# Optimization experiments

Measured on AMD Instinct MI355X. Metric: run time of the kernel, lower is better.

## Reference

```python
import jax, jax.numpy as jnp
import numpy as np

D_MODEL = 1024
NUM_HEADS = 16
D_HEAD = D_MODEL // NUM_HEADS


def setup_inputs() -> dict:
    key = jax.random.key(0)
    ks = jax.random.split(key, 5)
    B, T = 4, 2048
    x = jax.random.normal(ks[0], (B, T, D_MODEL), dtype=jnp.float32)
    s = 1.0 / np.sqrt(D_MODEL)
    # torch nn.Linear params: weight [out, in], bias [out]
    qkv_w = jax.random.uniform(ks[1], (3 * D_MODEL, D_MODEL), jnp.float32, -s, s)
    qkv_b = jax.random.uniform(ks[2], (3 * D_MODEL,), jnp.float32, -s, s)
    out_w = jax.random.uniform(ks[3], (D_MODEL, D_MODEL), jnp.float32, -s, s)
    out_b = jax.random.uniform(ks[4], (D_MODEL,), jnp.float32, -s, s)
    return {"x": x, "qkv_w": qkv_w, "qkv_b": qkv_b, "out_w": out_w, "out_b": out_b}


def reference(x, qkv_w, qkv_b, out_w, out_b):
    B, T, D = x.shape
    H, dh = NUM_HEADS, D_HEAD
    qkv = x @ qkv_w.T + qkv_b                      # [B,T,3D]
    q, k, v = jnp.split(qkv, 3, axis=-1)           # each [B,T,D]
    # split heads -> [B,H,T,dh]
    q = q.reshape(B, T, H, dh).transpose(0, 2, 1, 3)
    k = k.reshape(B, T, H, dh).transpose(0, 2, 1, 3)
    v = v.reshape(B, T, H, dh).transpose(0, 2, 1, 3)
    scores = jnp.einsum('bhqd,bhkd->bhqk', q, k) / jnp.sqrt(jnp.float32(dh))
    attn = jax.nn.softmax(scores, axis=-1)         # dropout p=0 (eval)
    out = jnp.einsum('bhqk,bhkd->bhqd', attn, v)   # [B,H,T,dh]
    out = out.transpose(0, 2, 1, 3).reshape(B, T, D)
    return out @ out_w.T + out_b
```

## Files before the change

### kernel.cpp

```cpp
#include <hip/hip_runtime.h>
#include <hip/hip_bf16.h>

typedef __bf16 bf16;
typedef __bf16 bf16x4 __attribute__((ext_vector_type(4)));
typedef __bf16 bf16x8 __attribute__((ext_vector_type(8)));
typedef float floatx4 __attribute__((ext_vector_type(4)));

#define MFMA16(a, b, c) __builtin_amdgcn_mfma_f32_16x16x32_bf16((a), (b), (c), 0, 0, 0)

constexpr int NHEADS = 16;

__device__ __forceinline__ void gld16(const bf16* g, bf16* l) {
  __builtin_amdgcn_global_load_lds(
      (const __attribute__((address_space(1))) void*)g,
      (__attribute__((address_space(3))) void*)l, 16, 0, 0);
}

__global__ __launch_bounds__(256) void cvt_bf16(const float* __restrict__ src,
                                                bf16* __restrict__ dst) {
  const int i = blockIdx.x * 256 + threadIdx.x;
  floatx4 a = ((const floatx4*)src)[2 * i];
  floatx4 b = ((const floatx4*)src)[2 * i + 1];
  bf16x8 o = {(bf16)a[0], (bf16)a[1], (bf16)a[2], (bf16)a[3],
              (bf16)b[0], (bf16)b[1], (bf16)b[2], (bf16)b[3]};
  ((bf16x8*)dst)[i] = o;
}

template <int MODE>
__global__ __launch_bounds__(256) void gemm_bt(
    const bf16* __restrict__ A, const bf16* __restrict__ W,
    const float* __restrict__ bias, bf16* __restrict__ out0,
    bf16* __restrict__ out1, bf16* __restrict__ out2,
    float* __restrict__ outf) {
  __shared__ __attribute__((aligned(16))) bf16 lds_a[128 * 32];
  __shared__ __attribute__((aligned(16))) bf16 lds_b[128 * 32];

  const int tid = threadIdx.x;
  const int wid = tid >> 6;
  const int lane = tid & 63;
  const int quad = lane >> 4;
  const int l16 = lane & 15;
  const int block_m = blockIdx.y * 128;
  const int block_n = blockIdx.x * 128;
  const int wm = (wid >> 1) * 64;
  const int wn = (wid & 1) * 64;

  floatx4 acc[4][4];
#pragma unroll
  for (int i = 0; i < 4; ++i)
#pragma unroll
    for (int j = 0; j < 4; ++j) acc[i][j] = (floatx4){0.f, 0.f, 0.f, 0.f};

  for (int k0 = 0; k0 < 1024; k0 += 32) {
#pragma unroll
    for (int i = 0; i < 2; ++i) {
      const int slot = wid * 128 + i * 64 + lane;
      const int row = slot >> 2;
      const int blk = slot & 3;
      const int lbase = (wid * 128 + i * 64) * 8;
      gld16(&A[(size_t)(block_m + row) * 1024 + k0 + blk * 8], &lds_a[lbase]);
      gld16(&W[(size_t)(block_n + row) * 1024 + k0 + blk * 8], &lds_b[lbase]);
    }
    __syncthreads();

    bf16x8 af[4], bf_[4];
#pragma unroll
    for (int mt = 0; mt < 4; ++mt)
      af[mt] = *(const bf16x8*)&lds_a[(wm + mt * 16 + l16) * 32 + quad * 8];
#pragma unroll
    for (int nt = 0; nt < 4; ++nt)
      bf_[nt] = *(const bf16x8*)&lds_b[(wn + nt * 16 + l16) * 32 + quad * 8];
#pragma unroll
    for (int mt = 0; mt < 4; ++mt)
#pragma unroll
      for (int nt = 0; nt < 4; ++nt)
        acc[mt][nt] = MFMA16(af[mt], bf_[nt], acc[mt][nt]);
    __syncthreads();
  }

#pragma unroll
  for (int nt = 0; nt < 4; ++nt) {
    const int n = block_n + wn + nt * 16 + l16;
    const float bv = bias[n];
#pragma unroll
    for (int mt = 0; mt < 4; ++mt) {
#pragma unroll
      for (int r = 0; r < 4; ++r) {
        const int m = block_m + wm + mt * 16 + quad * 4 + r;
        const float v = acc[mt][nt][r] + bv;
        if constexpr (MODE == 1) {
          outf[(size_t)m * 1024 + n] = v;
        } else {
          const int which = n >> 10;
          const int d = n & 1023;
          const int h = d >> 6;
          const int dd = d & 63;
          const int b = m >> 11;
          const int t = m & 2047;
          const size_t bh = (size_t)(b * NHEADS + h);
          if (which == 0)
            out0[(bh * 2048 + t) * 64 + dd] = (bf16)v;
          else if (which == 1)
            out1[(bh * 2048 + t) * 64 + dd] = (bf16)v;
          else
            out2[(bh * 64 + dd) * 2048 + t] = (bf16)v;
        }
      }
    }
  }
}

__global__ __launch_bounds__(256) void flash_attn(
    const bf16* __restrict__ q, const bf16* __restrict__ k,
    const bf16* __restrict__ vt, bf16* __restrict__ ctx) {
  __shared__ __attribute__((aligned(16))) bf16 k_lds[2][64 * 64];
  __shared__ __attribute__((aligned(16))) bf16 v_lds[2][64 * 64];
  __shared__ __attribute__((aligned(16))) bf16 p_lds[4][32][72];

  const int tid = threadIdx.x;
  const int wid = tid >> 6;
  const int lane = tid & 63;
  const int quad = lane >> 4;
  const int l16 = lane & 15;
  const int b = blockIdx.z;
  const int h = blockIdx.y;
  const int q0 = blockIdx.x * 128;
  const size_t bh = (size_t)(b * NHEADS + h);
  const bf16* qb = q + bh * 2048 * 64;
  const bf16* kb = k + bh * 2048 * 64;
  const bf16* vb = vt + bh * 64 * 2048;

  const bf16x8 ones = {(bf16)1.f, (bf16)1.f, (bf16)1.f, (bf16)1.f,
                       (bf16)1.f, (bf16)1.f, (bf16)1.f, (bf16)1.f};

  const int slot0 = wid * 128 + lane;
  const int slot1 = slot0 + 64;
  const int row0 = slot0 >> 3, c0 = (slot0 & 7) ^ (row0 & 7);
  const int row1 = slot1 >> 3, c1 = (slot1 & 7) ^ (row1 & 7);
  const bf16* kst0 = kb + (size_t)row0 * 64 + c0 * 8;
  const bf16* kst1 = kb + (size_t)row1 * 64 + c1 * 8;
  const bf16* vst0 = vb + (size_t)row0 * 2048 + c0 * 8;
  const bf16* vst1 = vb + (size_t)row1 * 2048 + c1 * 8;
  const int ldst0 = wid * 1024;
  const int ldst1 = wid * 1024 + 512;

  const int r7 = l16 & 7;
  const int ro = l16 * 64;
  const int sw0 = ro + ((quad ^ r7) * 8);
  const int sw1 = ro + (((quad + 4) ^ r7) * 8);

  bf16x8 qa[2][2];
#pragma unroll
  for (int s = 0; s < 2; ++s) {
    const int row = q0 + wid * 32 + s * 16 + l16;
    qa[s][0] = *(const bf16x8*)&qb[(size_t)row * 64 + quad * 8];
    qa[s][1] = *(const bf16x8*)&qb[(size_t)row * 64 + 32 + quad * 8];
  }

  floatx4 oacc[2][4];
  floatx4 lacc[2];
#pragma unroll
  for (int s = 0; s < 2; ++s) {
    lacc[s] = (floatx4){0.f, 0.f, 0.f, 0.f};
#pragma unroll
    for (int dt = 0; dt < 4; ++dt) oacc[s][dt] = (floatx4){0.f, 0.f, 0.f, 0.f};
  }

  gld16(kst0, &k_lds[0][ldst0]);
  gld16(kst1, &k_lds[0][ldst1]);
  gld16(vst0, &v_lds[0][ldst0]);
  gld16(vst1, &v_lds[0][ldst1]);
  __syncthreads();

  constexpr float L2E = 1.4426950408889634f;
  int cur = 0;
  for (int kt = 0; kt < 2048; kt += 64) {
    if (kt + 64 < 2048) {
      const int nb = cur ^ 1;
      gld16(kst0 + (size_t)(kt + 64) * 64, &k_lds[nb][ldst0]);
      gld16(kst1 + (size_t)(kt + 64) * 64, &k_lds[nb][ldst1]);
      gld16(vst0 + (kt + 64), &v_lds[nb][ldst0]);
      gld16(vst1 + (kt + 64), &v_lds[nb][ldst1]);
    }

    const bf16* kbuf = &k_lds[cur][0];
    const bf16* vbuf = &v_lds[cur][0];
    bf16x8 kf0[4], kf1[4], vf0[4], vf1[4];
#pragma unroll
    for (int nt = 0; nt < 4; ++nt) {
      kf0[nt] = *(const bf16x8*)&kbuf[nt * 1024 + sw0];
      kf1[nt] = *(const bf16x8*)&kbuf[nt * 1024 + sw1];
    }
#pragma unroll
    for (int dt = 0; dt < 4; ++dt) {
      vf0[dt] = *(const bf16x8*)&vbuf[dt * 1024 + sw0];
      vf1[dt] = *(const bf16x8*)&vbuf[dt * 1024 + sw1];
    }

#pragma unroll
    for (int s = 0; s < 2; ++s) {
      floatx4 st[4];
#pragma unroll
      for (int nt = 0; nt < 4; ++nt) {
        floatx4 a0 = (floatx4){0.f, 0.f, 0.f, 0.f};
        a0 = MFMA16(qa[s][0], kf0[nt], a0);
        st[nt] = MFMA16(qa[s][1], kf1[nt], a0);
      }
#pragma unroll
      for (int nt = 0; nt < 4; ++nt)
#pragma unroll
        for (int r = 0; r < 4; ++r) {
          const float p =
              __builtin_amdgcn_exp2f(fmaf(st[nt][r], 0.125f * L2E, -3.0f * L2E));
          p_lds[wid][s * 16 + quad * 4 + r][nt * 16 + l16] = (bf16)p;
        }
    }

#pragma unroll
    for (int s = 0; s < 2; ++s) {
      bf16x8 pa0 = *(const bf16x8*)&p_lds[wid][s * 16 + l16][quad * 8];
      bf16x8 pa1 = *(const bf16x8*)&p_lds[wid][s * 16 + l16][32 + quad * 8];
#pragma unroll
      for (int dt = 0; dt < 4; ++dt) {
        oacc[s][dt] = MFMA16(pa0, vf0[dt], oacc[s][dt]);
        oacc[s][dt] = MFMA16(pa1, vf1[dt], oacc[s][dt]);
      }
      lacc[s] = MFMA16(pa0, ones, lacc[s]);
      lacc[s] = MFMA16(pa1, ones, lacc[s]);
    }

    __syncthreads();
    cur ^= 1;
  }

#pragma unroll
  for (int s = 0; s < 2; ++s) {
    float linv[4];
#pragma unroll
    for (int r = 0; r < 4; ++r) linv[r] = 1.f / lacc[s][r];
    const size_t base =
        ((size_t)b * 2048 + q0 + wid * 32 + s * 16) * 1024 + h * 64;
#pragma unroll
    for (int dt = 0; dt < 4; ++dt)
#pragma unroll
      for (int r = 0; r < 4; ++r) {
        const float v = oacc[s][dt][r] * linv[r];
        ctx[base + (size_t)(quad * 4 + r) * 1024 + dt * 16 + l16] = (bf16)v;
      }
  }
}

extern "C" void kernel_launch(void* const* d_in, const int* in_sizes, int n_in,
                              void* d_out, int out_size, void* d_ws,
                              size_t ws_size, hipStream_t stream) {
  const float* x = (const float*)d_in[0];
  const float* qkv_w = (const float*)d_in[1];
  const float* qkv_b = (const float*)d_in[2];
  const float* out_w = (const float*)d_in[3];
  const float* out_b = (const float*)d_in[4];
  float* out = (float*)d_out;

  bf16* xb = (bf16*)d_out;

  bf16* ws = (bf16*)d_ws;
  const size_t SZ = (size_t)8192 * 1024;
  bf16* qkvwb = ws;
  bf16* outwb = qkvwb + 3072 * 1024;
  bf16* qws = outwb + 1024 * 1024;
  bf16* kws = qws + SZ;
  bf16* vtws = kws + SZ;
  bf16* ctx = vtws + SZ;

  cvt_bf16<<<4096, 256, 0, stream>>>(x, xb);
  cvt_bf16<<<1536, 256, 0, stream>>>(qkv_w, qkvwb);
  cvt_bf16<<<512, 256, 0, stream>>>(out_w, outwb);

  gemm_bt<0><<<dim3(24, 64), 256, 0, stream>>>(xb, qkvwb, qkv_b, qws, kws,
                                               vtws, nullptr);
  flash_attn<<<dim3(16, 16, 4), 256, 0, stream>>>(qws, kws, vtws, ctx);
  gemm_bt<1><<<dim3(8, 64), 256, 0, stream>>>(ctx, outwb, out_b, nullptr,
                                              nullptr, nullptr, out);
}
```

Measured before the change: 316.4 us.

## Triple-buffer K/V loads in flash attention and remap blocks for XCD locality

```diff
diff --git a/kernel.cpp b/kernel.cpp
--- a/kernel.cpp
+++ b/kernel.cpp
@@ -113,8 +113,8 @@
 __global__ __launch_bounds__(256) void flash_attn(
     const bf16* __restrict__ q, const bf16* __restrict__ k,
     const bf16* __restrict__ vt, bf16* __restrict__ ctx) {
-  __shared__ __attribute__((aligned(16))) bf16 k_lds[2][64 * 64];
-  __shared__ __attribute__((aligned(16))) bf16 v_lds[2][64 * 64];
+  __shared__ __attribute__((aligned(16))) bf16 k_lds[3][64 * 64];
+  __shared__ __attribute__((aligned(16))) bf16 v_lds[3][64 * 64];
   __shared__ __attribute__((aligned(16))) bf16 p_lds[4][32][72];
 
   const int tid = threadIdx.x;
@@ -122,9 +122,12 @@
   const int lane = tid & 63;
   const int quad = lane >> 4;
   const int l16 = lane & 15;
-  const int b = blockIdx.z;
-  const int h = blockIdx.y;
-  const int q0 = blockIdx.x * 128;
+
+  const int wg = blockIdx.x;
+  const int nl = (wg & 7) * 128 + (wg >> 3);
+  const int q0 = (nl & 15) * 128;
+  const int h = (nl >> 4) & 15;
+  const int b = nl >> 8;
   const size_t bh = (size_t)(b * NHEADS + h);
   const bf16* qb = q + bh * 2048 * 64;
   const bf16* kb = k + bh * 2048 * 64;
@@ -170,18 +173,34 @@
   gld16(kst1, &k_lds[0][ldst1]);
   gld16(vst0, &v_lds[0][ldst0]);
   gld16(vst1, &v_lds[0][ldst1]);
-  __syncthreads();
+  gld16(kst0 + (size_t)64 * 64, &k_lds[1][ldst0]);
+  gld16(kst1 + (size_t)64 * 64, &k_lds[1][ldst1]);
+  gld16(vst0 + 64, &v_lds[1][ldst0]);
+  gld16(vst1 + 64, &v_lds[1][ldst1]);
 
   constexpr float L2E = 1.4426950408889634f;
-  int cur = 0;
-  for (int kt = 0; kt < 2048; kt += 64) {
-    if (kt + 64 < 2048) {
-      const int nb = cur ^ 1;
-      gld16(kst0 + (size_t)(kt + 64) * 64, &k_lds[nb][ldst0]);
-      gld16(kst1 + (size_t)(kt + 64) * 64, &k_lds[nb][ldst1]);
-      gld16(vst0 + (kt + 64), &v_lds[nb][ldst0]);
-      gld16(vst1 + (kt + 64), &v_lds[nb][ldst1]);
-    }
+  for (int t = 0; t < 32; ++t) {
+    const int kt = t * 64;
+    const int cur = t % 3;
+    if (t + 2 < 32) {
+      const int nb = (t + 2) % 3;
+      const size_t ko = (size_t)(kt + 128) * 64;
+      gld16(kst0 + ko, &k_lds[nb][ldst0]);
+      gld16(kst1 + ko, &k_lds[nb][ldst1]);
+      gld16(vst0 + (kt + 128), &v_lds[nb][ldst0]);
+      gld16(vst1 + (kt + 128), &v_lds[nb][ldst1]);
+    }
+
+    if (t < 30) {
+      asm volatile("s_waitcnt vmcnt(8)" ::: "memory");
+    } else if (t == 30) {
+      asm volatile("s_waitcnt vmcnt(4)" ::: "memory");
+    } else {
+      asm volatile("s_waitcnt vmcnt(0)" ::: "memory");
+    }
+    __builtin_amdgcn_sched_barrier(0);
+    __builtin_amdgcn_s_barrier();
+    __builtin_amdgcn_sched_barrier(0);
 
     const bf16* kbuf = &k_lds[cur][0];
     const bf16* vbuf = &v_lds[cur][0];
@@ -229,8 +248,10 @@
       lacc[s] = MFMA16(pa1, ones, lacc[s]);
     }
 
-    __syncthreads();
-    cur ^= 1;
+    asm volatile("s_waitcnt lgkmcnt(0)" ::: "memory");
+    __builtin_amdgcn_sched_barrier(0);
+    __builtin_amdgcn_s_barrier();
+    __builtin_amdgcn_sched_barrier(0);
   }
 
 #pragma unroll
@@ -277,7 +298,7 @@
 
   gemm_bt<0><<<dim3(24, 64), 256, 0, stream>>>(xb, qkvwb, qkv_b, qws, kws,
                                                vtws, nullptr);
-  flash_attn<<<dim3(16, 16, 4), 256, 0, stream>>>(qws, kws, vtws, ctx);
+  flash_attn<<<1024, 256, 0, stream>>>(qws, kws, vtws, ctx);
   gemm_bt<1><<<dim3(8, 64), 256, 0, stream>>>(ctx, outwb, out_b, nullptr,
                                               nullptr, nullptr, out);
 }
```

Result: no change. 322.1 us (+1.8%).
